# Optimization experiments

Measured on AMD Instinct MI355X. Metric: run time of the kernel, lower is better.

## Reference

```python
import jax, jax.numpy as jnp
import numpy as np

SENTINEL = 1 << 20  # fill value for padded unique rows; far outside real coord range


def setup_inputs() -> dict:
    key = jax.random.key(0)
    k1, k2, k3, k4, k5, kw = jax.random.split(key, 6)
    M, C = 400000, 128
    voxel_features = jax.random.normal(k1, (M, C), dtype=jnp.float32)
    # coords: (batch_idx, z, y, x)
    b = jax.random.randint(k2, (M, 1), 0, 4, dtype=jnp.int32)
    z = jax.random.randint(k3, (M, 1), 0, 40, dtype=jnp.int32)
    y = jax.random.randint(k4, (M, 1), 0, 1024, dtype=jnp.int32)
    x = jax.random.randint(k5, (M, 1), 0, 1024, dtype=jnp.int32)
    voxel_coords = jnp.concatenate([b, z, y, x], axis=1)
    # layer-1 (stride=1) uses a random (in,out) matmul weight in the original;
    # materialize it as a fixed parameter for determinism.
    W0 = jax.random.normal(kw, (C, C), dtype=jnp.float32)
    return {"voxel_features": voxel_features, "voxel_coords": voxel_coords,
            "W0": W0, "batch_size": 4}


def _forward(voxel_features, W0, voxel_coords):
    M = voxel_features.shape[0]
    # layer 1: stride=1 -> relu then matmul (placeholder dense path)
    feats = jnp.maximum(voxel_features, 0.0) @ W0  # (M, 128)
    coords = voxel_coords
    # layers 2 and 3: stride=2 -> quantize coords (ALL 4 cols, incl. batch idx,
    # matching the original), unique, scatter-add features, relu
    for _ in range(2):
        coords = jnp.floor(coords.astype(jnp.float32) / 2.0).astype(jnp.int32)
        uniq, inv = jnp.unique(coords, axis=0, return_inverse=True,
                               size=M, fill_value=SENTINEL)
        inv = inv.reshape(-1)
        feats = jax.ops.segment_sum(feats, inv, num_segments=M)  # fused scatter-add
        feats = jnp.maximum(feats, 0.0)
        coords = uniq
    # rows beyond the true unique count are zero padding (sentinel coords)
    return feats


def reference(voxel_features, voxel_coords, W0, batch_size):
    return _forward(voxel_features, W0, voxel_coords)
```

## Files before the change

### kernel.cpp

```cpp
#include <hip/hip_runtime.h>
#include <stdint.h>

#define C 128

typedef __attribute__((ext_vector_type(8))) short bf16x8;
typedef __attribute__((ext_vector_type(4))) float f32x4;
typedef __attribute__((ext_vector_type(2))) float f32x2;

__device__ __forceinline__ uint32_t f2bf1(float f) {
    uint32_t u = __float_as_uint(f);
    return (u + 0x7FFFu + ((u >> 16) & 1u)) >> 16;
}


__global__ __launch_bounds__(512) void zeroconv_kernel(
    uint4* __restrict__ zbase, int nquads,
    const float* __restrict__ W, ushort* __restrict__ Wt, int nzb) {
    int b = blockIdx.x, t = threadIdx.x;
    if (b < nzb) {
        int i = b * 512 + t;
        if (i < nquads) zbase[i] = (uint4){0u, 0u, 0u, 0u};
    } else {
        int id = (b - nzb) * 512 + t;
        int n = id >> 7, k = id & 127;
        Wt[id] = (ushort)f2bf1(W[k * C + n]);
    }
}

__global__ __launch_bounds__(512) void mark_kernel(
    const int* __restrict__ coords, uint32_t* __restrict__ bm1,
    uint32_t* __restrict__ bm2, int M) {
    int i = blockIdx.x * 512 + threadIdx.x;
    if (i >= M) return;
    int4 c = ((const int4*)coords)[i];
    uint32_t k1 = ((uint32_t)(c.x>>1)<<23) | ((uint32_t)(c.y>>1)<<18) |
                  ((uint32_t)(c.z>>1)<<9)  | (uint32_t)(c.w>>1);
    uint32_t k2 = ((uint32_t)(c.y>>2)<<16) | ((uint32_t)(c.z>>2)<<8) | (uint32_t)(c.w>>2);
    atomicOr(&bm1[k1>>5], 1u << (k1 & 31));
    atomicOr(&bm2[k2>>5], 1u << (k2 & 31));
}

__device__ __forceinline__ void bscan1_512(const uint32_t* bm, uint32_t* bs,
                                           int blk, uint32_t* s, int t) {
    int base = blk * 1024 + t * 2;
    uint32_t sum = __popc(bm[base]) + __popc(bm[base+1]);
    s[t] = sum;
    __syncthreads();
    for (int off = 256; off > 0; off >>= 1) {
        if (t < off) s[t] += s[t + off];
        __syncthreads();
    }
    if (t == 0) bs[blk] = s[0];
}

__device__ __forceinline__ void bscan3_512(const uint32_t* bm, const uint32_t* bs,
                                           uint32_t* wp, int blk, uint32_t* s, int t) {
    int base = blk * 1024 + t * 2;
    uint32_t p0 = __popc(bm[base]), p1 = __popc(bm[base+1]);
    uint32_t sum = p0 + p1;
    s[t] = sum;
    __syncthreads();
    for (int off = 1; off < 512; off <<= 1) {
        uint32_t add = (t >= off) ? s[t - off] : 0u;
        __syncthreads();
        s[t] += add;
        __syncthreads();
    }
    uint32_t ex = s[t] - sum + bs[blk];
    wp[base]   = ex;
    wp[base+1] = ex + p0;
}

__device__ __forceinline__ void blksum_scan_512(uint32_t* bs, uint32_t* total,
                                                int nb, uint32_t* s, int t) {
    uint32_t v = (t < nb) ? bs[t] : 0u;
    s[t] = v;
    __syncthreads();
    for (int off = 1; off < 512; off <<= 1) {
        uint32_t add = (t >= off) ? s[t - off] : 0u;
        __syncthreads();
        s[t] += add;
        __syncthreads();
    }
    if (t < nb) bs[t] = s[t] - v;
    if (t == nb - 1) *total = s[t];
}

__device__ __forceinline__ void vscan1_512(const uint32_t* v, uint32_t* bs,
                                           int blk, int n, uint32_t* s, int t) {
    int base = blk * 1024 + t * 2;
    uint32_t sum = 0;
    if (base     < n) sum += v[base];
    if (base + 1 < n) sum += v[base+1];
    s[t] = sum;
    __syncthreads();
    for (int off = 256; off > 0; off >>= 1) {
        if (t < off) s[t] += s[t + off];
        __syncthreads();
    }
    if (t == 0) bs[blk] = s[0];
}

__device__ __forceinline__ void vscan3_512(const uint32_t* v, const uint32_t* bs,
                                           uint32_t* ex_out, int blk, int n,
                                           uint32_t* s, int t) {
    int base = blk * 1024 + t * 2;
    uint32_t p0 = (base     < n) ? v[base]   : 0u;
    uint32_t p1 = (base + 1 < n) ? v[base+1] : 0u;
    uint32_t sum = p0 + p1;
    s[t] = sum;
    __syncthreads();
    for (int off = 1; off < 512; off <<= 1) {
        uint32_t add = (t >= off) ? s[t - off] : 0u;
        __syncthreads();
        s[t] += add;
        __syncthreads();
    }
    uint32_t e = s[t] - sum + bs[blk];
    if (base     < n) ex_out[base]   = e;
    if (base + 1 < n) ex_out[base+1] = e + p0;
}

__global__ __launch_bounds__(512) void mscan1_kernel(
    const uint32_t* __restrict__ bm1, uint32_t* __restrict__ bs1,
    const uint32_t* __restrict__ bm2, uint32_t* __restrict__ bs2) {
    __shared__ uint32_t s[512];
    int b = blockIdx.x, t = threadIdx.x;
    if (b < 512) bscan1_512(bm1, bs1, b, s, t);
    else         bscan1_512(bm2, bs2, b - 512, s, t);
}

__global__ __launch_bounds__(512) void mscan2_kernel(
    uint32_t* __restrict__ bs1, uint32_t* __restrict__ bs2,
    uint32_t* __restrict__ totals) {
    __shared__ uint32_t s[512];
    int t = threadIdx.x;
    if (blockIdx.x == 0) blksum_scan_512(bs1, &totals[0], 512, s, t);
    else                 blksum_scan_512(bs2, &totals[1], 32,  s, t);
}

__global__ __launch_bounds__(512) void mscan3_kernel(
    const uint32_t* __restrict__ bm1, const uint32_t* __restrict__ bs1,
    uint32_t* __restrict__ wp1,
    const uint32_t* __restrict__ bm2, const uint32_t* __restrict__ bs2,
    uint32_t* __restrict__ wp2) {
    __shared__ uint32_t s[512];
    int b = blockIdx.x, t = threadIdx.x;
    if (b < 512) bscan3_512(bm1, bs1, wp1, b, s, t);
    else         bscan3_512(bm2, bs2, wp2, b - 512, s, t);
}

__global__ __launch_bounds__(512) void count_kernel(
    const int* __restrict__ coords, const uint32_t* __restrict__ bm1,
    const uint32_t* __restrict__ wp1, uint32_t* __restrict__ counts,
    uint32_t* __restrict__ rank1_arr, uint32_t* __restrict__ slot1, int M) {
    int i = blockIdx.x * 512 + threadIdx.x;
    if (i >= M) return;
    int4 c = ((const int4*)coords)[i];
    uint32_t k1 = ((uint32_t)(c.x>>1)<<23) | ((uint32_t)(c.y>>1)<<18) |
                  ((uint32_t)(c.z>>1)<<9)  | (uint32_t)(c.w>>1);
    uint32_t r1 = wp1[k1>>5] + __popc(bm1[k1>>5] & ((1u << (k1 & 31)) - 1u));
    rank1_arr[i] = r1;
    slot1[i] = atomicAdd(&counts[r1], 1u);
}

__global__ __launch_bounds__(512) void mk1_kernel(
    const uint32_t* __restrict__ counts, uint32_t* __restrict__ bsc,
    const uint32_t* __restrict__ bm1, const uint32_t* __restrict__ wp1,
    const uint32_t* __restrict__ bm2, const uint32_t* __restrict__ wp2,
    uint32_t* __restrict__ parent_r2, uint32_t* __restrict__ rowcounts2,
    uint32_t* __restrict__ childbase, int M, int nbc, int nwords) {
    int b = blockIdx.x, t = threadIdx.x;
    if (b < nbc) {
        __shared__ uint32_t s[512];
        vscan1_512(counts, bsc, b, M, s, t);
        return;
    }
    int w = (b - nbc) * 512 + t;
    if (w >= nwords) return;
    uint32_t bits = bm1[w];
    if (!bits) return;
    uint32_t r1 = wp1[w];
    while (bits) {
        int bit = __ffs(bits) - 1;
        uint32_t k1 = ((uint32_t)w << 5) | (uint32_t)bit;
        uint32_t z1 = (k1 >> 18) & 31u, y1 = (k1 >> 9) & 511u, x1 = k1 & 511u;
        uint32_t k2 = ((z1 >> 1) << 16) | ((y1 >> 1) << 8) | (x1 >> 1);
        uint32_t word2 = bm2[k2 >> 5];
        uint32_t r2 = wp2[k2 >> 5] + __popc(word2 & ((1u << (k2 & 31)) - 1u));
        parent_r2[r1] = r2;
        childbase[r1] = atomicAdd(&rowcounts2[r2], counts[r1]);
        r1++;
        bits &= bits - 1;
    }
}

__global__ __launch_bounds__(512) void mk2_kernel(
    uint32_t* __restrict__ bsc, uint32_t* __restrict__ totals,
    const uint32_t* __restrict__ rowcounts2, uint32_t* __restrict__ bsc2,
    int M, int nbc) {
    __shared__ uint32_t s[512];
    int b = blockIdx.x, t = threadIdx.x;
    if (b == 0) blksum_scan_512(bsc, &totals[2], nbc, s, t);
    else        vscan1_512(rowcounts2, bsc2, b - 1, M, s, t);
}

__global__ __launch_bounds__(512) void mk3_kernel(
    const uint32_t* __restrict__ counts, const uint32_t* __restrict__ bsc,
    uint32_t* __restrict__ start1,
    uint32_t* __restrict__ bsc2, uint32_t* __restrict__ totals,
    int M, int nbc) {
    __shared__ uint32_t s[512];
    int b = blockIdx.x, t = threadIdx.x;
    if (b < nbc) vscan3_512(counts, bsc, start1, b, M, s, t);
    else         blksum_scan_512(bsc2, &totals[3], nbc, s, t);
}

__global__ __launch_bounds__(512) void mk4_kernel(
    const uint32_t* __restrict__ rank1_arr, const uint32_t* __restrict__ start1,
    const uint32_t* __restrict__ slot1, uint32_t* __restrict__ perm,
    const uint32_t* __restrict__ rowcounts2, const uint32_t* __restrict__ bsc2,
    uint32_t* __restrict__ rowstart2, int M, int npb, int nbc) {
    int b = blockIdx.x, t = threadIdx.x;
    if (b < npb) {
        int i = b * 512 + t;
        if (i >= M) return;
        uint32_t r1 = rank1_arr[i];
        perm[start1[r1] + slot1[i]] = i;
        return;
    }
    __shared__ uint32_t s[512];
    vscan3_512(rowcounts2, bsc2, rowstart2, b - npb, M, s, t);
}

__device__ __forceinline__ void gemm_loadX(const float* __restrict__ X,
                                           int tile, int lm, int kg, f32x4* pf) {
    const char* xb = (const char*)X + ((size_t)tile*16 + lm)*512 + kg*32;
    #pragma unroll
    for (int ks = 0; ks < 4; ++ks) {
        pf[2*ks]   = __builtin_nontemporal_load((const f32x4*)(xb + ks*128));
        pf[2*ks+1] = __builtin_nontemporal_load((const f32x4*)(xb + ks*128 + 16));
    }
}

__device__ __forceinline__ void gemm_compute(const f32x4* pf, const char* wbase,
                                             ushort* __restrict__ g, int tile,
                                             int lm, int kg) {
    bf16x8 af[4];
    #pragma unroll
    for (int ks = 0; ks < 4; ++ks) {
        f32x4 a = pf[2*ks], b = pf[2*ks+1];
        union { uint32_t u[4]; bf16x8 v; } cv;
        cv.u[0] = f2bf1(fmaxf(a[0],0.f)) | (f2bf1(fmaxf(a[1],0.f)) << 16);
        cv.u[1] = f2bf1(fmaxf(a[2],0.f)) | (f2bf1(fmaxf(a[3],0.f)) << 16);
        cv.u[2] = f2bf1(fmaxf(b[0],0.f)) | (f2bf1(fmaxf(b[1],0.f)) << 16);
        cv.u[3] = f2bf1(fmaxf(b[2],0.f)) | (f2bf1(fmaxf(b[3],0.f)) << 16);
        af[ks] = cv.v;
    }
    ushort* grow = g + (size_t)((size_t)tile*16 + 4*kg)*128 + lm;
    #pragma unroll
    for (int n = 0; n < 8; ++n) {
        bf16x8 b0 = *(const bf16x8*)(wbase + n*256);
        bf16x8 b1 = *(const bf16x8*)(wbase + n*256 + 8192);
        bf16x8 b2 = *(const bf16x8*)(wbase + n*256 + 16384);
        bf16x8 b3 = *(const bf16x8*)(wbase + n*256 + 24576);
        f32x4 acc = (f32x4){0.f, 0.f, 0.f, 0.f};
        acc = __builtin_amdgcn_mfma_f32_16x16x32_bf16(af[0], b0, acc, 0, 0, 0);
        acc = __builtin_amdgcn_mfma_f32_16x16x32_bf16(af[1], b1, acc, 0, 0, 0);
        acc = __builtin_amdgcn_mfma_f32_16x16x32_bf16(af[2], b2, acc, 0, 0, 0);
        acc = __builtin_amdgcn_mfma_f32_16x16x32_bf16(af[3], b3, acc, 0, 0, 0);
        #pragma unroll
        for (int r = 0; r < 4; ++r)
            grow[(size_t)r*128 + 16*n] = (ushort)f2bf1(acc[r]);
    }
}

__global__ __launch_bounds__(256) void gemmflat_kernel(
    const float* __restrict__ X, const ushort* __restrict__ Wt,
    ushort* __restrict__ g, int M, int nflat, int ngemm,
    const uint32_t* __restrict__ parent_r2, const uint32_t* __restrict__ counts,
    const uint32_t* __restrict__ start1, const uint32_t* __restrict__ rowstart2,
    const uint32_t* __restrict__ childbase, const uint32_t* __restrict__ perm,
    uint32_t* __restrict__ perm_f, const uint32_t* __restrict__ totals) {
    int b = blockIdx.x;
    const int t = threadIdx.x;
    if (b < nflat) {
        int i = b * 256 + t;
        if (i >= M) return;
        uint32_t U1 = totals[0];
        if ((uint32_t)i >= U1) return;
        uint32_t r2 = parent_r2[i];
        uint32_t cnt = counts[i];
        uint32_t dst = rowstart2[r2] + childbase[i];
        uint32_t s = start1[i];
        perm_f[dst] = perm[s] | 0x80000000u;
        for (uint32_t q = 1; q < cnt; ++q) perm_f[dst + q] = perm[s + q];
        return;
    }
    __shared__ __align__(16) ushort wlds[16384];
    const int gb = b - nflat;
    {
        int sm = t & 15, kc = t >> 4;
        const char* src = (const char*)Wt;
        char* dst = (char*)wlds;
        #pragma unroll
        for (int n = 0; n < 8; ++n) {
            uint4 v = *(const uint4*)(src + n*4096 + sm*256 + kc*16);
            *(uint4*)(dst + (kc>>2)*8192 + (kc&3)*2048 + n*256 + sm*16) = v;
        }
    }
    __syncthreads();
    const int l = t & 63;
    const int lm = l & 15, kg = l >> 4;
    const int ntiles = M >> 4;
    const int nw = ngemm * 4;
    int tile = gb * 4 + (t >> 6);
    const char* wbase = (const char*)wlds + kg*2048 + lm*16;

    f32x4 pfA[8], pfB[8];
    if (tile < ntiles)      gemm_loadX(X, tile, lm, kg, pfA);
    if (tile + nw < ntiles) gemm_loadX(X, tile + nw, lm, kg, pfB);
    while (true) {
        if (tile >= ntiles) break;
        gemm_compute(pfA, wbase, g, tile, lm, kg);
        if (tile + 2*nw < ntiles) gemm_loadX(X, tile + 2*nw, lm, kg, pfA);
        tile += nw;
        if (tile >= ntiles) break;
        gemm_compute(pfB, wbase, g, tile, lm, kg);
        if (tile + 2*nw < ntiles) gemm_loadX(X, tile + 2*nw, lm, kg, pfB);
        tile += nw;
    }
}

__global__ __launch_bounds__(256) void gather2_kernel(
    const uint32_t* __restrict__ rowstart2, const uint32_t* __restrict__ rowcounts2,
    const uint32_t* __restrict__ perm_f, const ushort* __restrict__ g,
    float* __restrict__ out, int M) {
    int wid = (blockIdx.x * 256 + threadIdx.x) >> 6;
    wid = __builtin_amdgcn_readfirstlane(wid);
    int lane = threadIdx.x & 63;
    if (wid >= M) return;
    const uint32_t* G = (const uint32_t*)g;
    float accx = 0.f, accy = 0.f;
    uint32_t n = rowcounts2[wid];
    if (n) {
        uint32_t s = rowstart2[wid];
        uint32_t ev = (lane < (int)n) ? perm_f[s + lane] : 0u;
        float sx = 0.f, sy = 0.f;
        uint32_t ecur = (uint32_t)__shfl((int)ev, 0);
        uint32_t pk = G[(size_t)(ecur & 0x7FFFFFFFu) * 64 + lane];
        for (uint32_t q = 1; q < n; ++q) {
            uint32_t en = (q < 64u) ? (uint32_t)__shfl((int)ev, (int)q)
                                    : perm_f[s + q];
            uint32_t pkn = G[(size_t)(en & 0x7FFFFFFFu) * 64 + lane];
            sx += __uint_as_float(pk << 16);
            sy += __uint_as_float(pk & 0xFFFF0000u);
            if (en >> 31) {
                accx += fmaxf(sx, 0.f); accy += fmaxf(sy, 0.f);
                sx = 0.f; sy = 0.f;
            }
            pk = pkn;
        }
        sx += __uint_as_float(pk << 16);
        sy += __uint_as_float(pk & 0xFFFF0000u);
        accx += fmaxf(sx, 0.f);
        accy += fmaxf(sy, 0.f);
    }
    f32x2 o; o[0] = accx; o[1] = accy;
    __builtin_nontemporal_store(o, (f32x2*)out + (size_t)wid * 64 + lane);
}

extern "C" void kernel_launch(void* const* d_in, const int* in_sizes, int n_in,
                              void* d_out, int out_size, void* d_ws, size_t ws_size,
                              hipStream_t stream) {
    const float* X      = (const float*)d_in[0];
    const int*   coords = (const int*)d_in[1];
    const float* W      = (const float*)d_in[2];
    const int M = in_sizes[0] / C;

    const int NW1 = 1 << 19;
    const int NW2 = 1 << 15;
    const int NBC = (M + 1023) / 1024;
    const int NPB = (M + 511) / 512;
    const int NF  = (M + 255) / 256;
    const int NGEMM = 1280;

    char* ws = (char*)d_ws;
    size_t off = 0;
    ushort*   g         = (ushort*)(ws + off);   off += (size_t)M * C * 2;
    uint32_t* bm1       = (uint32_t*)(ws + off); off += (size_t)NW1 * 4;
    uint32_t* bm2       = (uint32_t*)(ws + off); off += (size_t)NW2 * 4;
    uint32_t* counts    = (uint32_t*)(ws + off); off += (size_t)M * 4;
    uint32_t* rowcounts2= (uint32_t*)(ws + off); off += (size_t)M * 4;
    const size_t zero_off   = (size_t)M * C * 2;
    const size_t zero_bytes = off - zero_off;
    uint32_t* wp1       = (uint32_t*)(ws + off); off += (size_t)NW1 * 4;
    uint32_t* wp2       = (uint32_t*)(ws + off); off += (size_t)NW2 * 4;
    uint32_t* bs1       = (uint32_t*)(ws + off); off += 512 * 4;
    uint32_t* bs2       = (uint32_t*)(ws + off); off += 512 * 4;
    uint32_t* bsc       = (uint32_t*)(ws + off); off += 512 * 4;
    uint32_t* bsc2      = (uint32_t*)(ws + off); off += 512 * 4;
    uint32_t* totals    = (uint32_t*)(ws + off); off += 4 * 4;
    uint32_t* start1    = (uint32_t*)(ws + off); off += (size_t)M * 4;
    uint32_t* rank1_arr = (uint32_t*)(ws + off); off += (size_t)M * 4;
    uint32_t* slot1     = (uint32_t*)(ws + off); off += (size_t)M * 4;
    uint32_t* perm      = (uint32_t*)(ws + off); off += (size_t)M * 4;
    uint32_t* parent_r2 = (uint32_t*)(ws + off); off += (size_t)M * 4;
    uint32_t* childbase = (uint32_t*)(ws + off); off += (size_t)M * 4;
    uint32_t* rowstart2 = (uint32_t*)(ws + off); off += (size_t)M * 4;
    ushort*   Wt        = (ushort*)(ws + off);   off += (size_t)C * C * 2;
    uint32_t* perm_f    = rank1_arr;

    const int NQ  = (int)(zero_bytes / 16);
    const int NZB = (NQ + 511) / 512;

    zeroconv_kernel<<<NZB + 32, 512, 0, stream>>>((uint4*)(ws + zero_off), NQ, W, Wt, NZB);
    mark_kernel<<<NPB, 512, 0, stream>>>(coords, bm1, bm2, M);
    mscan1_kernel<<<544, 512, 0, stream>>>(bm1, bs1, bm2, bs2);
    mscan2_kernel<<<2, 512, 0, stream>>>(bs1, bs2, totals);
    mscan3_kernel<<<544, 512, 0, stream>>>(bm1, bs1, wp1, bm2, bs2, wp2);
    count_kernel<<<NPB, 512, 0, stream>>>(coords, bm1, wp1, counts, rank1_arr, slot1, M);
    mk1_kernel<<<NBC + NW1/512, 512, 0, stream>>>(counts, bsc, bm1, wp1, bm2, wp2,
                                                  parent_r2, rowcounts2, childbase,
                                                  M, NBC, NW1);
    mk2_kernel<<<1 + NBC, 512, 0, stream>>>(bsc, totals, rowcounts2, bsc2, M, NBC);
    mk3_kernel<<<NBC + 1, 512, 0, stream>>>(counts, bsc, start1, bsc2, totals, M, NBC);
    mk4_kernel<<<NPB + NBC, 512, 0, stream>>>(rank1_arr, start1, slot1, perm,
                                              rowcounts2, bsc2, rowstart2, M, NPB, NBC);
    gemmflat_kernel<<<NF + NGEMM, 256, 0, stream>>>(X, Wt, g, M, NF, NGEMM,
                                                    parent_r2, counts, start1, rowstart2,
                                                    childbase, perm, perm_f, totals);
    gather2_kernel<<<(M + 3) / 4, 256, 0, stream>>>(
        rowstart2, rowcounts2, perm_f, g, (float*)d_out, M);
}
```

Measured before the change: 246.8 us.

## Fuse preprocessing kernels into one persistent kernel with grid barriers alongside GEMM

Replaces the chain of nine small preprocessing launches (mark, scans, count, mk1-4, flatten) with one persistent kernel. 384 blocks run the phases in sequence and sync through atomic software grid barriers, while the remaining blocks run the bf16 GEMM concurrently in the same launch. This removes per-launch overhead and gaps between the small dependent kernels, and overlaps index building with the GEMM. The risks are deadlock if the prep blocks are not all co-resident, fewer blocks left for the GEMM, and barrier spin cost.

```diff
diff --git a/kernel.cpp b/kernel.cpp
--- a/kernel.cpp
+++ b/kernel.cpp
@@ -2,6 +2,7 @@
 #include <stdint.h>
 
 #define C 128
+#define NPREP 384
 
 typedef __attribute__((ext_vector_type(8))) short bf16x8;
 typedef __attribute__((ext_vector_type(4))) float f32x4;
@@ -27,40 +28,41 @@
     }
 }
 
-__global__ __launch_bounds__(512) void mark_kernel(
-    const int* __restrict__ coords, uint32_t* __restrict__ bm1,
-    uint32_t* __restrict__ bm2, int M) {
-    int i = blockIdx.x * 512 + threadIdx.x;
-    if (i >= M) return;
-    int4 c = ((const int4*)coords)[i];
-    uint32_t k1 = ((uint32_t)(c.x>>1)<<23) | ((uint32_t)(c.y>>1)<<18) |
-                  ((uint32_t)(c.z>>1)<<9)  | (uint32_t)(c.w>>1);
-    uint32_t k2 = ((uint32_t)(c.y>>2)<<16) | ((uint32_t)(c.z>>2)<<8) | (uint32_t)(c.w>>2);
-    atomicOr(&bm1[k1>>5], 1u << (k1 & 31));
-    atomicOr(&bm2[k2>>5], 1u << (k2 & 31));
-}
-
-__device__ __forceinline__ void bscan1_512(const uint32_t* bm, uint32_t* bs,
+__device__ __forceinline__ void prep_barrier(uint32_t* bars, int phase) {
+    __syncthreads();
+    if (threadIdx.x == 0) {
+        __hip_atomic_fetch_add(&bars[phase], 1u, __ATOMIC_RELEASE,
+                               __HIP_MEMORY_SCOPE_AGENT);
+        while (__hip_atomic_load(&bars[phase], __ATOMIC_ACQUIRE,
+                                 __HIP_MEMORY_SCOPE_AGENT) < (uint32_t)NPREP)
+            __builtin_amdgcn_s_sleep(8);
+    }
+    __syncthreads();
+}
+
+__device__ __forceinline__ void bscan1_256(const uint32_t* bm, uint32_t* bs,
                                            int blk, uint32_t* s, int t) {
-    int base = blk * 1024 + t * 2;
-    uint32_t sum = __popc(bm[base]) + __popc(bm[base+1]);
+    int base = blk * 1024 + t * 4;
+    uint32_t sum = __popc(bm[base]) + __popc(bm[base+1]) +
+                   __popc(bm[base+2]) + __popc(bm[base+3]);
     s[t] = sum;
     __syncthreads();
-    for (int off = 256; off > 0; off >>= 1) {
+    for (int off = 128; off > 0; off >>= 1) {
         if (t < off) s[t] += s[t + off];
         __syncthreads();
     }
     if (t == 0) bs[blk] = s[0];
 }
 
-__device__ __forceinline__ void bscan3_512(const uint32_t* bm, const uint32_t* bs,
+__device__ __forceinline__ void bscan3_256(const uint32_t* bm, const uint32_t* bs,
                                            uint32_t* wp, int blk, uint32_t* s, int t) {
-    int base = blk * 1024 + t * 2;
-    uint32_t p0 = __popc(bm[base]), p1 = __popc(bm[base+1]);
-    uint32_t sum = p0 + p1;
+    int base = blk * 1024 + t * 4;
+    uint32_t p0 = __popc(bm[base]),   p1 = __popc(bm[base+1]);
+    uint32_t p2 = __popc(bm[base+2]), p3 = __popc(bm[base+3]);
+    uint32_t sum = p0 + p1 + p2 + p3;
     s[t] = sum;
     __syncthreads();
-    for (int off = 1; off < 512; off <<= 1) {
+    for (int off = 1; off < 256; off <<= 1) {
         uint32_t add = (t >= off) ? s[t - off] : 0u;
         __syncthreads();
         s[t] += add;
@@ -69,168 +71,66 @@
     uint32_t ex = s[t] - sum + bs[blk];
     wp[base]   = ex;
     wp[base+1] = ex + p0;
-}
-
-__device__ __forceinline__ void blksum_scan_512(uint32_t* bs, uint32_t* total,
-                                                int nb, uint32_t* s, int t) {
-    uint32_t v = (t < nb) ? bs[t] : 0u;
-    s[t] = v;
-    __syncthreads();
-    for (int off = 1; off < 512; off <<= 1) {
-        uint32_t add = (t >= off) ? s[t - off] : 0u;
-        __syncthreads();
-        s[t] += add;
-        __syncthreads();
-    }
-    if (t < nb) bs[t] = s[t] - v;
-    if (t == nb - 1) *total = s[t];
-}
-
-__device__ __forceinline__ void vscan1_512(const uint32_t* v, uint32_t* bs,
+    wp[base+2] = ex + p0 + p1;
+    wp[base+3] = ex + p0 + p1 + p2;
+}
+
+__device__ __forceinline__ void vscan1_256(const uint32_t* v, uint32_t* bs,
                                            int blk, int n, uint32_t* s, int t) {
-    int base = blk * 1024 + t * 2;
+    int base = blk * 1024 + t * 4;
     uint32_t sum = 0;
-    if (base     < n) sum += v[base];
-    if (base + 1 < n) sum += v[base+1];
+    #pragma unroll
+    for (int j = 0; j < 4; j++) sum += (base + j < n) ? v[base + j] : 0u;
     s[t] = sum;
     __syncthreads();
-    for (int off = 256; off > 0; off >>= 1) {
+    for (int off = 128; off > 0; off >>= 1) {
         if (t < off) s[t] += s[t + off];
         __syncthreads();
     }
     if (t == 0) bs[blk] = s[0];
 }
 
-__device__ __forceinline__ void vscan3_512(const uint32_t* v, const uint32_t* bs,
+__device__ __forceinline__ void vscan3_256(const uint32_t* v, const uint32_t* bs,
                                            uint32_t* ex_out, int blk, int n,
                                            uint32_t* s, int t) {
-    int base = blk * 1024 + t * 2;
-    uint32_t p0 = (base     < n) ? v[base]   : 0u;
-    uint32_t p1 = (base + 1 < n) ? v[base+1] : 0u;
-    uint32_t sum = p0 + p1;
+    int base = blk * 1024 + t * 4;
+    uint32_t p[4];
+    #pragma unroll
+    for (int j = 0; j < 4; j++) p[j] = (base + j < n) ? v[base + j] : 0u;
+    uint32_t sum = p[0] + p[1] + p[2] + p[3];
     s[t] = sum;
     __syncthreads();
-    for (int off = 1; off < 512; off <<= 1) {
+    for (int off = 1; off < 256; off <<= 1) {
         uint32_t add = (t >= off) ? s[t - off] : 0u;
         __syncthreads();
         s[t] += add;
         __syncthreads();
     }
     uint32_t e = s[t] - sum + bs[blk];
-    if (base     < n) ex_out[base]   = e;
-    if (base + 1 < n) ex_out[base+1] = e + p0;
-}
-
-__global__ __launch_bounds__(512) void mscan1_kernel(
-    const uint32_t* __restrict__ bm1, uint32_t* __restrict__ bs1,
-    const uint32_t* __restrict__ bm2, uint32_t* __restrict__ bs2) {
-    __shared__ uint32_t s[512];
-    int b = blockIdx.x, t = threadIdx.x;
-    if (b < 512) bscan1_512(bm1, bs1, b, s, t);
-    else         bscan1_512(bm2, bs2, b - 512, s, t);
-}
-
-__global__ __launch_bounds__(512) void mscan2_kernel(
-    uint32_t* __restrict__ bs1, uint32_t* __restrict__ bs2,
-    uint32_t* __restrict__ totals) {
-    __shared__ uint32_t s[512];
-    int t = threadIdx.x;
-    if (blockIdx.x == 0) blksum_scan_512(bs1, &totals[0], 512, s, t);
-    else                 blksum_scan_512(bs2, &totals[1], 32,  s, t);
-}
-
-__global__ __launch_bounds__(512) void mscan3_kernel(
-    const uint32_t* __restrict__ bm1, const uint32_t* __restrict__ bs1,
-    uint32_t* __restrict__ wp1,
-    const uint32_t* __restrict__ bm2, const uint32_t* __restrict__ bs2,
-    uint32_t* __restrict__ wp2) {
-    __shared__ uint32_t s[512];
-    int b = blockIdx.x, t = threadIdx.x;
-    if (b < 512) bscan3_512(bm1, bs1, wp1, b, s, t);
-    else         bscan3_512(bm2, bs2, wp2, b - 512, s, t);
-}
-
-__global__ __launch_bounds__(512) void count_kernel(
-    const int* __restrict__ coords, const uint32_t* __restrict__ bm1,
-    const uint32_t* __restrict__ wp1, uint32_t* __restrict__ counts,
-    uint32_t* __restrict__ rank1_arr, uint32_t* __restrict__ slot1, int M) {
-    int i = blockIdx.x * 512 + threadIdx.x;
-    if (i >= M) return;
-    int4 c = ((const int4*)coords)[i];
-    uint32_t k1 = ((uint32_t)(c.x>>1)<<23) | ((uint32_t)(c.y>>1)<<18) |
-                  ((uint32_t)(c.z>>1)<<9)  | (uint32_t)(c.w>>1);
-    uint32_t r1 = wp1[k1>>5] + __popc(bm1[k1>>5] & ((1u << (k1 & 31)) - 1u));
-    rank1_arr[i] = r1;
-    slot1[i] = atomicAdd(&counts[r1], 1u);
-}
-
-__global__ __launch_bounds__(512) void mk1_kernel(
-    const uint32_t* __restrict__ counts, uint32_t* __restrict__ bsc,
-    const uint32_t* __restrict__ bm1, const uint32_t* __restrict__ wp1,
-    const uint32_t* __restrict__ bm2, const uint32_t* __restrict__ wp2,
-    uint32_t* __restrict__ parent_r2, uint32_t* __restrict__ rowcounts2,
-    uint32_t* __restrict__ childbase, int M, int nbc, int nwords) {
-    int b = blockIdx.x, t = threadIdx.x;
-    if (b < nbc) {
-        __shared__ uint32_t s[512];
-        vscan1_512(counts, bsc, b, M, s, t);
-        return;
-    }
-    int w = (b - nbc) * 512 + t;
-    if (w >= nwords) return;
-    uint32_t bits = bm1[w];
-    if (!bits) return;
-    uint32_t r1 = wp1[w];
-    while (bits) {
-        int bit = __ffs(bits) - 1;
-        uint32_t k1 = ((uint32_t)w << 5) | (uint32_t)bit;
-        uint32_t z1 = (k1 >> 18) & 31u, y1 = (k1 >> 9) & 511u, x1 = k1 & 511u;
-        uint32_t k2 = ((z1 >> 1) << 16) | ((y1 >> 1) << 8) | (x1 >> 1);
-        uint32_t word2 = bm2[k2 >> 5];
-        uint32_t r2 = wp2[k2 >> 5] + __popc(word2 & ((1u << (k2 & 31)) - 1u));
-        parent_r2[r1] = r2;
-        childbase[r1] = atomicAdd(&rowcounts2[r2], counts[r1]);
-        r1++;
-        bits &= bits - 1;
-    }
-}
-
-__global__ __launch_bounds__(512) void mk2_kernel(
-    uint32_t* __restrict__ bsc, uint32_t* __restrict__ totals,
-    const uint32_t* __restrict__ rowcounts2, uint32_t* __restrict__ bsc2,
-    int M, int nbc) {
-    __shared__ uint32_t s[512];
-    int b = blockIdx.x, t = threadIdx.x;
-    if (b == 0) blksum_scan_512(bsc, &totals[2], nbc, s, t);
-    else        vscan1_512(rowcounts2, bsc2, b - 1, M, s, t);
-}
-
-__global__ __launch_bounds__(512) void mk3_kernel(
-    const uint32_t* __restrict__ counts, const uint32_t* __restrict__ bsc,
-    uint32_t* __restrict__ start1,
-    uint32_t* __restrict__ bsc2, uint32_t* __restrict__ totals,
-    int M, int nbc) {
-    __shared__ uint32_t s[512];
-    int b = blockIdx.x, t = threadIdx.x;
-    if (b < nbc) vscan3_512(counts, bsc, start1, b, M, s, t);
-    else         blksum_scan_512(bsc2, &totals[3], nbc, s, t);
-}
-
-__global__ __launch_bounds__(512) void mk4_kernel(
-    const uint32_t* __restrict__ rank1_arr, const uint32_t* __restrict__ start1,
-    const uint32_t* __restrict__ slot1, uint32_t* __restrict__ perm,
-    const uint32_t* __restrict__ rowcounts2, const uint32_t* __restrict__ bsc2,
-    uint32_t* __restrict__ rowstart2, int M, int npb, int nbc) {
-    int b = blockIdx.x, t = threadIdx.x;
-    if (b < npb) {
-        int i = b * 512 + t;
-        if (i >= M) return;
-        uint32_t r1 = rank1_arr[i];
-        perm[start1[r1] + slot1[i]] = i;
-        return;
-    }
-    __shared__ uint32_t s[512];
-    vscan3_512(rowcounts2, bsc2, rowstart2, b - npb, M, s, t);
+    #pragma unroll
+    for (int j = 0; j < 4; j++) {
+        if (base + j < n) ex_out[base + j] = e;
+        e += p[j];
+    }
+}
+
+__device__ __forceinline__ void blksum_scan_256(uint32_t* bs, uint32_t* total,
+                                                int nb, uint32_t* s, int t) {
+    uint32_t v0 = (2*t     < nb) ? bs[2*t]     : 0u;
+    uint32_t v1 = (2*t + 1 < nb) ? bs[2*t + 1] : 0u;
+    uint32_t sum = v0 + v1;
+    s[t] = sum;
+    __syncthreads();
+    for (int off = 1; off < 256; off <<= 1) {
+        uint32_t add = (t >= off) ? s[t - off] : 0u;
+        __syncthreads();
+        s[t] += add;
+        __syncthreads();
+    }
+    uint32_t ex = s[t] - sum;
+    if (2*t     < nb) bs[2*t]     = ex;
+    if (2*t + 1 < nb) bs[2*t + 1] = ex + v0;
+    if (t == 255 && total) *total = s[255];
 }
 
 __device__ __forceinline__ void gemm_loadX(const float* __restrict__ X,
@@ -275,38 +175,16 @@
     }
 }
 
-__global__ __launch_bounds__(256) void gemmflat_kernel(
-    const float* __restrict__ X, const ushort* __restrict__ Wt,
-    ushort* __restrict__ g, int M, int nflat, int ngemm,
-    const uint32_t* __restrict__ parent_r2, const uint32_t* __restrict__ counts,
-    const uint32_t* __restrict__ start1, const uint32_t* __restrict__ rowstart2,
-    const uint32_t* __restrict__ childbase, const uint32_t* __restrict__ perm,
-    uint32_t* __restrict__ perm_f, const uint32_t* __restrict__ totals) {
-    int b = blockIdx.x;
+__device__ void gemm_role(const float* __restrict__ X, const ushort* __restrict__ Wt,
+                          ushort* __restrict__ g, char* smem, int gb, int ngemm, int M) {
     const int t = threadIdx.x;
-    if (b < nflat) {
-        int i = b * 256 + t;
-        if (i >= M) return;
-        uint32_t U1 = totals[0];
-        if ((uint32_t)i >= U1) return;
-        uint32_t r2 = parent_r2[i];
-        uint32_t cnt = counts[i];
-        uint32_t dst = rowstart2[r2] + childbase[i];
-        uint32_t s = start1[i];
-        perm_f[dst] = perm[s] | 0x80000000u;
-        for (uint32_t q = 1; q < cnt; ++q) perm_f[dst + q] = perm[s + q];
-        return;
-    }
-    __shared__ __align__(16) ushort wlds[16384];
-    const int gb = b - nflat;
     {
         int sm = t & 15, kc = t >> 4;
         const char* src = (const char*)Wt;
-        char* dst = (char*)wlds;
         #pragma unroll
         for (int n = 0; n < 8; ++n) {
             uint4 v = *(const uint4*)(src + n*4096 + sm*256 + kc*16);
-            *(uint4*)(dst + (kc>>2)*8192 + (kc&3)*2048 + n*256 + sm*16) = v;
+            *(uint4*)(smem + (kc>>2)*8192 + (kc&3)*2048 + n*256 + sm*16) = v;
         }
     }
     __syncthreads();
@@ -315,7 +193,7 @@
     const int ntiles = M >> 4;
     const int nw = ngemm * 4;
     int tile = gb * 4 + (t >> 6);
-    const char* wbase = (const char*)wlds + kg*2048 + lm*16;
+    const char* wbase = smem + kg*2048 + lm*16;
 
     f32x4 pfA[8], pfB[8];
     if (tile < ntiles)      gemm_loadX(X, tile, lm, kg, pfA);
@@ -329,6 +207,110 @@
         gemm_compute(pfB, wbase, g, tile, lm, kg);
         if (tile + 2*nw < ntiles) gemm_loadX(X, tile + 2*nw, lm, kg, pfB);
         tile += nw;
+    }
+}
+
+__global__ __launch_bounds__(256) void fused_kernel(
+    const int* __restrict__ coords,
+    uint32_t* __restrict__ bm1, uint32_t* __restrict__ bm2,
+    uint32_t* __restrict__ bs1, uint32_t* __restrict__ bs2,
+    uint32_t* __restrict__ wp1, uint32_t* __restrict__ wp2,
+    uint32_t* __restrict__ totals, uint32_t* __restrict__ counts,
+    uint32_t* __restrict__ rank1_arr, uint32_t* __restrict__ slot1,
+    uint32_t* __restrict__ bsc, uint32_t* __restrict__ bsc2,
+    uint32_t* __restrict__ start1, uint32_t* __restrict__ parent_r2,
+    uint32_t* __restrict__ rowcounts2, uint32_t* __restrict__ childbase,
+    uint32_t* __restrict__ rowstart2, uint32_t* __restrict__ perm,
+    uint32_t* __restrict__ perm_f, uint32_t* __restrict__ bars,
+    const float* __restrict__ X, const ushort* __restrict__ Wt,
+    ushort* __restrict__ g, int M, int ngemm) {
+    __shared__ __align__(16) char smem[32768];
+    const int b = blockIdx.x, t = threadIdx.x;
+    if (b >= NPREP) { gemm_role(X, Wt, g, smem, b - NPREP, ngemm, M); return; }
+
+    uint32_t* s = (uint32_t*)smem;
+    const int NBC = (M + 1023) / 1024;
+    const int NW1 = 1 << 19;
+    const int STRD = NPREP * 256;
+
+    for (int i = b*256 + t; i < M; i += STRD) {
+        int4 c = ((const int4*)coords)[i];
+        uint32_t k1 = ((uint32_t)(c.x>>1)<<23) | ((uint32_t)(c.y>>1)<<18) |
+                      ((uint32_t)(c.z>>1)<<9)  | (uint32_t)(c.w>>1);
+        uint32_t k2 = ((uint32_t)(c.y>>2)<<16) | ((uint32_t)(c.z>>2)<<8) |
+                      (uint32_t)(c.w>>2);
+        atomicOr(&bm1[k1>>5], 1u << (k1 & 31));
+        atomicOr(&bm2[k2>>5], 1u << (k2 & 31));
+    }
+    prep_barrier(bars, 0);
+    for (int u = b; u < 544; u += NPREP) {
+        if (u < 512) bscan1_256(bm1, bs1, u, s, t);
+        else         bscan1_256(bm2, bs2, u - 512, s, t);
+    }
+    prep_barrier(bars, 1);
+    if (b == 0)      blksum_scan_256(bs1, &totals[0], 512, s, t);
+    else if (b == 1) blksum_scan_256(bs2, &totals[1], 32,  s, t);
+    prep_barrier(bars, 2);
+    for (int u = b; u < 544; u += NPREP) {
+        if (u < 512) bscan3_256(bm1, bs1, wp1, u, s, t);
+        else         bscan3_256(bm2, bs2, wp2, u - 512, s, t);
+    }
+    prep_barrier(bars, 3);
+    for (int i = b*256 + t; i < M; i += STRD) {
+        int4 c = ((const int4*)coords)[i];
+        uint32_t k1 = ((uint32_t)(c.x>>1)<<23) | ((uint32_t)(c.y>>1)<<18) |
+                      ((uint32_t)(c.z>>1)<<9)  | (uint32_t)(c.w>>1);
+        uint32_t r1 = wp1[k1>>5] + __popc(bm1[k1>>5] & ((1u << (k1 & 31)) - 1u));
+        rank1_arr[i] = r1;
+        slot1[i] = atomicAdd(&counts[r1], 1u);
+    }
+    prep_barrier(bars, 4);
+    for (int u = b; u < NBC + NW1/256; u += NPREP) {
+        if (u < NBC) { vscan1_256(counts, bsc, u, M, s, t); continue; }
+        int w = (u - NBC) * 256 + t;
+        uint32_t bits = bm1[w];
+        if (!bits) continue;
+        uint32_t r1 = wp1[w];
+        while (bits) {
+            int bit = __ffs(bits) - 1;
+            uint32_t k1 = ((uint32_t)w << 5) | (uint32_t)bit;
+            uint32_t z1 = (k1 >> 18) & 31u, y1 = (k1 >> 9) & 511u, x1 = k1 & 511u;
+            uint32_t k2 = ((z1 >> 1) << 16) | ((y1 >> 1) << 8) | (x1 >> 1);
+            uint32_t word2 = bm2[k2 >> 5];
+            uint32_t r2 = wp2[k2 >> 5] + __popc(word2 & ((1u << (k2 & 31)) - 1u));
+            parent_r2[r1] = r2;
+            childbase[r1] = atomicAdd(&rowcounts2[r2], counts[r1]);
+            r1++;
+            bits &= bits - 1;
+        }
+    }
+    prep_barrier(bars, 5);
+    for (int u = b; u < 1 + NBC; u += NPREP) {
+        if (u == 0) blksum_scan_256(bsc, &totals[2], NBC, s, t);
+        else        vscan1_256(rowcounts2, bsc2, u - 1, M, s, t);
+    }
+    prep_barrier(bars, 6);
+    for (int u = b; u < NBC + 1; u += NPREP) {
+        if (u < NBC) vscan3_256(counts, bsc, start1, u, M, s, t);
+        else         blksum_scan_256(bsc2, &totals[3], NBC, s, t);
+    }
+    prep_barrier(bars, 7);
+    for (int u = b; u < NBC; u += NPREP)
+        vscan3_256(rowcounts2, bsc2, rowstart2, u, M, s, t);
+    for (int i = b*256 + t; i < M; i += STRD) {
+        uint32_t r1 = rank1_arr[i];
+        perm[start1[r1] + slot1[i]] = i;
+    }
+    prep_barrier(bars, 8);
+    uint32_t U1 = totals[0];
+    for (int i = b*256 + t; i < M; i += STRD) {
+        if ((uint32_t)i >= U1) break;
+        uint32_t r2 = parent_r2[i];
+        uint32_t cnt = counts[i];
+        uint32_t dst = rowstart2[r2] + childbase[i];
+        uint32_t sp = start1[i];
+        perm_f[dst] = perm[sp] | 0x80000000u;
+        for (uint32_t q = 1; q < cnt; ++q) perm_f[dst + q] = perm[sp + q];
     }
 }
 
@@ -380,10 +362,7 @@
 
     const int NW1 = 1 << 19;
     const int NW2 = 1 << 15;
-    const int NBC = (M + 1023) / 1024;
-    const int NPB = (M + 511) / 512;
-    const int NF  = (M + 255) / 256;
-    const int NGEMM = 1280;
+    const int NGEMM = 1280 - NPREP;
 
     char* ws = (char*)d_ws;
     size_t off = 0;
@@ -392,6 +371,7 @@
     uint32_t* bm2       = (uint32_t*)(ws + off); off += (size_t)NW2 * 4;
     uint32_t* counts    = (uint32_t*)(ws + off); off += (size_t)M * 4;
     uint32_t* rowcounts2= (uint32_t*)(ws + off); off += (size_t)M * 4;
+    uint32_t* bars      = (uint32_t*)(ws + off); off += 16 * 4;
     const size_t zero_off   = (size_t)M * C * 2;
     const size_t zero_bytes = off - zero_off;
     uint32_t* wp1       = (uint32_t*)(ws + off); off += (size_t)NW1 * 4;
@@ -415,21 +395,10 @@
     const int NZB = (NQ + 511) / 512;
 
     zeroconv_kernel<<<NZB + 32, 512, 0, stream>>>((uint4*)(ws + zero_off), NQ, W, Wt, NZB);
-    mark_kernel<<<NPB, 512, 0, stream>>>(coords, bm1, bm2, M);
-    mscan1_kernel<<<544, 512, 0, stream>>>(bm1, bs1, bm2, bs2);
-    mscan2_kernel<<<2, 512, 0, stream>>>(bs1, bs2, totals);
-    mscan3_kernel<<<544, 512, 0, stream>>>(bm1, bs1, wp1, bm2, bs2, wp2);
-    count_kernel<<<NPB, 512, 0, stream>>>(coords, bm1, wp1, counts, rank1_arr, slot1, M);
-    mk1_kernel<<<NBC + NW1/512, 512, 0, stream>>>(counts, bsc, bm1, wp1, bm2, wp2,
-                                                  parent_r2, rowcounts2, childbase,
-                                                  M, NBC, NW1);
-    mk2_kernel<<<1 + NBC, 512, 0, stream>>>(bsc, totals, rowcounts2, bsc2, M, NBC);
-    mk3_kernel<<<NBC + 1, 512, 0, stream>>>(counts, bsc, start1, bsc2, totals, M, NBC);
-    mk4_kernel<<<NPB + NBC, 512, 0, stream>>>(rank1_arr, start1, slot1, perm,
-                                              rowcounts2, bsc2, rowstart2, M, NPB, NBC);
-    gemmflat_kernel<<<NF + NGEMM, 256, 0, stream>>>(X, Wt, g, M, NF, NGEMM,
-                                                    parent_r2, counts, start1, rowstart2,
-                                                    childbase, perm, perm_f, totals);
+    fused_kernel<<<NPREP + NGEMM, 256, 0, stream>>>(
+        coords, bm1, bm2, bs1, bs2, wp1, wp2, totals, counts, rank1_arr, slot1,
+        bsc, bsc2, start1, parent_r2, rowcounts2, childbase, rowstart2, perm,
+        perm_f, bars, X, Wt, g, M, NGEMM);
     gather2_kernel<<<(M + 3) / 4, 256, 0, stream>>>(
         rowstart2, rowcounts2, perm_f, g, (float*)d_out, M);
 }
```

Result: slower. 836.2 us (+238.8%).
